# Optimization experiments

Hardware: AMD Instinct MI355X
Metric: run time of the kernel (lower is better)

## Reference

```python
import jax, jax.numpy as jnp
import numpy as np

H = 16  # n_heads
EPS = 1e-12  # F.normalize eps


def _l2norm(x):
    n = jnp.sqrt(jnp.sum(x * x, axis=-1, keepdims=True))
    return x / jnp.maximum(n, EPS)


def setup_inputs() -> dict:
    key = jax.random.key(0)
    ks = jax.random.split(key, 10)
    bs, S, dim = 2, 2048, 2048
    dh = dim // H
    x = jax.random.normal(ks[0], (bs, S, dim), dtype=jnp.float32)
    mask = jnp.ones((bs, S, S), dtype=jnp.int32)  # mask==0 would be masked out
    s = 0.02
    Wq = jax.random.normal(ks[1], (dim, dim), jnp.float32) * s
    bq = jax.random.normal(ks[2], (dim,), jnp.float32) * s
    Wk = jax.random.normal(ks[3], (dim, dim), jnp.float32) * s
    bk = jax.random.normal(ks[4], (dim,), jnp.float32) * s
    Wv = jax.random.normal(ks[5], (dim, dim), jnp.float32) * s
    bv = jax.random.normal(ks[6], (dim,), jnp.float32) * s
    Wo = jax.random.normal(ks[7], (dim, dim), jnp.float32) * s
    bo = jax.random.normal(ks[8], (dim,), jnp.float32) * s
    attention_scale = jnp.asarray(1.0 / np.sqrt(dh), dtype=jnp.float32)
    return {"x": x, "mask": mask, "Wq": Wq, "bq": bq, "Wk": Wk, "bk": bk,
            "Wv": Wv, "bv": bv, "Wo": Wo, "bo": bo,
            "attention_scale": attention_scale}


def reference(x, mask, Wq, bq, Wk, bk, Wv, bv, Wo, bo, attention_scale):
    bs, S, dim = x.shape
    dh = dim // H

    def split_heads(t):  # [bs,S,dim] -> [bs,H,S,dh]
        return t.reshape(bs, S, H, dh).transpose(0, 2, 1, 3)

    q = split_heads(x @ Wq.T + bq)
    k = split_heads(x @ Wk.T + bk)
    v = split_heads(x @ Wv.T + bv)

    # normalized attention: L2-normalize q,k then learned scale on q
    q = _l2norm(q) * attention_scale
    k = _l2norm(k)

    scores = jnp.einsum('bhqd,bhkd->bhqk', q, k)
    masked = mask[:, None, :, :] == 0  # broadcast over heads
    scores = jnp.where(masked, -jnp.inf, scores)
    weights = jax.nn.softmax(scores.astype(jnp.float32), axis=-1).astype(scores.dtype)
    # dropout p=0.0 -> identity
    ctx = jnp.einsum('bhqk,bhkd->bhqd', weights, v)
    ctx = ctx.transpose(0, 2, 1, 3).reshape(bs, S, dim)
    return ctx @ Wo.T + bo
```

## Files before the change

### kernel.cpp

```cpp
#include <hip/hip_runtime.h>
#include <hip/hip_bf16.h>
#include <stdint.h>

typedef __attribute__((ext_vector_type(8))) short short8;
typedef __attribute__((ext_vector_type(4))) float f32x4;
typedef __attribute__((ext_vector_type(4))) unsigned short ushort4v;
typedef __attribute__((ext_vector_type(4))) float float4v;
typedef __attribute__((ext_vector_type(4))) int int4v;

#define GLL16(gp, lp)                                                        \
  __builtin_amdgcn_global_load_lds(                                          \
      (const __attribute__((address_space(1))) void*)(gp),                   \
      (__attribute__((address_space(3))) void*)(lp), 16, 0, 0)

__device__ __forceinline__ unsigned short f2bf(float f) {
  union { float f; unsigned u; } v; v.f = f;
  unsigned r = v.u + 0x7FFFu + ((v.u >> 16) & 1u);
  return (unsigned short)(r >> 16);
}
__device__ __forceinline__ float bf2f(unsigned short h) {
  union { unsigned u; float f; } v; v.u = ((unsigned)h) << 16;
  return v.f;
}
__device__ __forceinline__ unsigned pkbf(float a, float b) {
  union { __hip_bfloat162 h; unsigned u; } v;
  v.h = __float22bfloat162_rn(make_float2(a, b));
  return v.u;
}

__global__ __launch_bounds__(256) void cast_kernel(
    const float* __restrict__ x, const float* __restrict__ Wq,
    const float* __restrict__ Wk, const float* __restrict__ Wv,
    const float* __restrict__ Wo, const float* __restrict__ bq,
    const float* __restrict__ bk, const float* __restrict__ bv,
    unsigned short* __restrict__ xb, unsigned short* __restrict__ wqkv,
    unsigned short* __restrict__ wob, float* __restrict__ biasq) {
  const int X4 = 2097152, W4 = 1048576;
  const int total = X4 + 4 * W4 + 1536;
  for (int i = blockIdx.x * 256 + threadIdx.x; i < total; i += gridDim.x * 256) {
    if (i < X4 + 4 * W4) {
      const float* src; unsigned short* dst;
      if (i < X4) { src = x + (size_t)i * 4; dst = xb + (size_t)i * 4; }
      else {
        int j = i - X4;
        if (j < 3 * W4) {
          const float* w = (j < W4) ? Wq : (j < 2 * W4 ? Wk : Wv);
          int j0 = (j < W4) ? j : (j < 2 * W4 ? j - W4 : j - 2 * W4);
          src = w + (size_t)j0 * 4; dst = wqkv + (size_t)j * 4;
        } else {
          int j0 = j - 3 * W4; src = Wo + (size_t)j0 * 4; dst = wob + (size_t)j0 * 4;
        }
      }
      float4v v = *(const float4v*)src;
      ushort4v o; o.x = f2bf(v.x); o.y = f2bf(v.y); o.z = f2bf(v.z); o.w = f2bf(v.w);
      *(ushort4v*)dst = o;
    } else {
      int j = i - (X4 + 4 * W4);
      const float* src = (j < 512) ? bq + j * 4
                        : (j < 1024 ? bk + (j - 512) * 4 : bv + (j - 1024) * 4);
      *(float4v*)(biasq + j * 4) = *(const float4v*)src;
    }
  }
}

__global__ __launch_bounds__(256) void maskflag_kernel(const int* __restrict__ mask,
                                                       int* __restrict__ flags) {
  const int bid = blockIdx.x;
  const int b = bid >> 9, qt = (bid >> 5) & 15, kt = bid & 31;
  const int t = threadIdx.x;
  const int* mb = mask + (size_t)b * 4194304;
  int ok = 1;
#pragma unroll
  for (int j = 0; j < 8; ++j) {
    int flat = t * 32 + j * 4;
    int r = flat >> 6, c = flat & 63;
    int4v v = *(const int4v*)(mb + (size_t)(qt * 128 + r) * 2048 + kt * 64 + c);
    ok &= (v.x != 0) & (v.y != 0) & (v.z != 0) & (v.w != 0);
  }
  int all = __syncthreads_and(ok);
  if (t == 0) flags[bid] = all;
}

template <bool OUT_BF16>
__global__ __launch_bounds__(256) void gemm_bt(
    const unsigned short* __restrict__ A, const unsigned short* __restrict__ B,
    void* __restrict__ C, const float* __restrict__ bias, int N, int K) {
  __shared__ unsigned short As[128 * 64];
  __shared__ unsigned short Bs[128 * 64];
  const int tid = threadIdx.x, lane = tid & 63;
  const int wid = __builtin_amdgcn_readfirstlane(tid >> 6);
  const int wr = wid >> 1, wc = wid & 1;
  const int bm = blockIdx.y, bn = blockIdx.x;
  const int g = lane >> 4, q15 = lane & 15;
  f32x4 acc[4][4];
#pragma unroll
  for (int i = 0; i < 4; ++i)
#pragma unroll
    for (int j = 0; j < 4; ++j) acc[i][j] = f32x4{0.f, 0.f, 0.f, 0.f};
  const size_t ldab = (size_t)K * 2;
  const int nkt = K >> 6;
  for (int kt = 0; kt < nkt; ++kt) {
#pragma unroll
    for (int i = 0; i < 4; ++i) {
      int c = i * 4 + wid;
      int o = c * 1024 + lane * 16;
      int row = o >> 7, colb = o & 127;
      GLL16((const char*)A + (size_t)(bm * 128 + row) * ldab + kt * 128 + colb,
            (char*)As + c * 1024);
      GLL16((const char*)B + (size_t)(bn * 128 + row) * ldab + kt * 128 + colb,
            (char*)Bs + c * 1024);
    }
    __syncthreads();
#pragma unroll
    for (int kk = 0; kk < 2; ++kk) {
      short8 af[4], bfv[4];
#pragma unroll
      for (int mf = 0; mf < 4; ++mf)
        af[mf] = *(const short8*)((const char*)As +
                 (wr * 64 + mf * 16 + q15) * 128 + kk * 64 + g * 16);
#pragma unroll
      for (int nf = 0; nf < 4; ++nf)
        bfv[nf] = *(const short8*)((const char*)Bs +
                  (wc * 64 + nf * 16 + q15) * 128 + kk * 64 + g * 16);
#pragma unroll
      for (int mf = 0; mf < 4; ++mf)
#pragma unroll
        for (int nf = 0; nf < 4; ++nf)
          acc[mf][nf] = __builtin_amdgcn_mfma_f32_16x16x32_bf16(
              af[mf], bfv[nf], acc[mf][nf], 0, 0, 0);
    }
    __syncthreads();
  }
#pragma unroll
  for (int nf = 0; nf < 4; ++nf) {
    int col = bn * 128 + wc * 64 + nf * 16 + q15;
    float bv = bias[col];
#pragma unroll
    for (int mf = 0; mf < 4; ++mf) {
#pragma unroll
      for (int r = 0; r < 4; ++r) {
        int row = bm * 128 + wr * 64 + mf * 16 + g * 4 + r;
        float v = acc[mf][nf][r] + bv;
        if (OUT_BF16)
          ((unsigned short*)C)[(size_t)row * N + col] = f2bf(v);
        else
          ((float*)C)[(size_t)row * N + col] = v;
      }
    }
  }
}

__global__ __launch_bounds__(256) void norm_vt_kernel(
    unsigned short* __restrict__ QKV, unsigned short* __restrict__ VT,
    const float* __restrict__ scale_p) {
  __shared__ unsigned short vt[128 * 72];
  const int bid = blockIdx.x;
  const int b = bid >> 9, h = (bid >> 5) & 15, st = bid & 31;
  const int t = threadIdx.x;
  const int r = t >> 2, qd = t & 3;
  const float scale = scale_p[0] * 1.4426950408889634f;
  unsigned short* rowp = QKV + (size_t)(b * 2048 + st * 64 + r) * 6144;
#pragma unroll
  for (int part = 0; part < 2; ++part) {
    unsigned short* p = rowp + part * 2048 + h * 128 + qd * 32;
    short8 v[4];
    float ss = 0.f;
#pragma unroll
    for (int j = 0; j < 4; ++j) {
      v[j] = *(const short8*)(p + j * 8);
#pragma unroll
      for (int e = 0; e < 8; ++e) {
        float f = bf2f((unsigned short)v[j][e]);
        ss += f * f;
      }
    }
    ss += __shfl_xor(ss, 1, 64);
    ss += __shfl_xor(ss, 2, 64);
    float inv = 1.0f / fmaxf(sqrtf(ss), 1e-12f);
    if (part == 0) inv *= scale;
#pragma unroll
    for (int j = 0; j < 4; ++j) {
      short8 w;
#pragma unroll
      for (int e = 0; e < 8; ++e)
        w[e] = (short)f2bf(bf2f((unsigned short)v[j][e]) * inv);
      *(short8*)(p + j * 8) = w;
    }
  }
  {
    const unsigned short* p = rowp + 4096 + h * 128 + qd * 32;
#pragma unroll
    for (int j = 0; j < 4; ++j) {
      short8 v = *(const short8*)(p + j * 8);
#pragma unroll
      for (int e = 0; e < 8; ++e) {
        int d = qd * 32 + j * 8 + e;
        vt[d * 72 + r] = (unsigned short)v[e];
      }
    }
  }
  __syncthreads();
  {
    const int d = t >> 1, half = t & 1;
    unsigned short* dst = VT + ((size_t)(b * 16 + h) * 128 + d) * 2048 + st * 64 + half * 32;
#pragma unroll
    for (int j = 0; j < 4; ++j)
      *(short8*)(dst + j * 8) = *(const short8*)(&vt[d * 72 + half * 32 + j * 8]);
  }
}

__global__ __launch_bounds__(512, 4) void flash_kernel(
    const unsigned short* __restrict__ QKV, const unsigned short* __restrict__ VT,
    const int* __restrict__ flags, const int* __restrict__ mask,
    unsigned short* __restrict__ ctx) {
  __shared__ char lds[65536];
  const int tid = threadIdx.x, lane = tid & 63;
  const int wid = __builtin_amdgcn_readfirstlane(tid >> 6);
  const int g = lane >> 4, q15 = lane & 15;
  const int bid = blockIdx.x;
  const int b = bid >> 8, h = (bid >> 4) & 15, qt = bid & 15;

  unsigned fb = 0;
#pragma unroll 1
  for (int i = 0; i < 32; ++i)
    fb |= (unsigned)(flags[b * 512 + qt * 32 + i] != 0) << i;

  short8 qf[4];
  {
    const char* qbase = (const char*)QKV +
        (size_t)(b * 2048 + qt * 128 + wid * 16 + q15) * 12288 + h * 256;
#pragma unroll
    for (int kk = 0; kk < 4; ++kk)
      qf[kk] = *(const short8*)(qbase + kk * 64 + g * 16);
  }

  const char* sptr;
  size_t sbase[4]; int ldso[4]; size_t kstep;
  if (wid < 4) {
    sptr = (const char*)QKV; kstep = (size_t)64 * 12288;
#pragma unroll
    for (int i = 0; i < 4; ++i) {
      int c = wid * 4 + i;
      int row = c * 4 + g;
      int scol = ((lane & 15) * 16) ^ ((row & 7) << 4);
      sbase[i] = (size_t)(b * 2048 + row) * 12288 + 4096 + h * 256 + scol;
      ldso[i] = c * 1024;
    }
  } else {
    sptr = (const char*)VT; kstep = 128;
#pragma unroll
    for (int i = 0; i < 4; ++i) {
      int c2 = (wid - 4) * 4 + i;
      int d = c2 * 8 + (lane >> 3);
      int scol = ((lane & 7) * 16) ^ ((d & 7) << 4);
      sbase[i] = ((size_t)((b * 16 + h) * 128 + d)) * 4096 + scol;
      ldso[i] = 16384 + c2 * 1024;
    }
  }

  f32x4 o[8];
#pragma unroll
  for (int i = 0; i < 8; ++i) o[i] = f32x4{0.f, 0.f, 0.f, 0.f};
  float mrun = -1e30f, lrun = 0.f;
  const int l0 = q15 + 16 * ((2 * g) & 3), l1 = l0 + 16;
  const bool hi = ((g >> 1) & 1) != 0;

#pragma unroll
  for (int i = 0; i < 4; ++i) GLL16(sptr + sbase[i], lds + ldso[i]);
  __syncthreads();

  for (int kt = 0; kt < 32; ++kt) {
    const int cur = kt & 1;
    if (kt < 31) {
#pragma unroll
      for (int i = 0; i < 4; ++i)
        GLL16(sptr + sbase[i] + (size_t)(kt + 1) * kstep,
              lds + (cur ^ 1) * 32768 + ldso[i]);
    }
    const char* Ks = lds + cur * 32768;
    const char* Vs = Ks + 16384;

    f32x4 s[4];
#pragma unroll
    for (int nf = 0; nf < 4; ++nf) s[nf] = f32x4{0.f, 0.f, 0.f, 0.f};
#pragma unroll
    for (int nf = 0; nf < 4; ++nf) {
      const char* kb = Ks + (nf * 16 + q15) * 256;
      const int sw = (q15 & 7) << 4;
#pragma unroll
      for (int kk = 0; kk < 4; ++kk) {
        short8 kf = *(const short8*)(kb + ((kk * 64 + g * 16) ^ sw));
        s[nf] = __builtin_amdgcn_mfma_f32_16x16x32_bf16(kf, qf[kk], s[nf], 0, 0, 0);
      }
    }

    if (!((fb >> kt) & 1)) {
#pragma unroll
      for (int nf = 0; nf < 4; ++nf)
#pragma unroll
        for (int r = 0; r < 4; ++r) {
          int key = kt * 64 + nf * 16 + g * 4 + r;
          int q = qt * 128 + wid * 16 + q15;
          if (mask[(size_t)b * 4194304 + (size_t)q * 2048 + key] == 0)
            s[nf][r] = -__builtin_inff();
        }
    }

    float pmax = s[0][0];
#pragma unroll
    for (int nf = 0; nf < 4; ++nf)
#pragma unroll
      for (int r = 0; r < 4; ++r) pmax = fmaxf(pmax, s[nf][r]);
    pmax = fmaxf(pmax, __shfl_xor(pmax, 16, 64));
    pmax = fmaxf(pmax, __shfl_xor(pmax, 32, 64));

    if (__any(pmax - mrun > 8.0f)) {
      float mnew = fmaxf(mrun, pmax);
      float sc = exp2f(mrun - mnew);
      mrun = mnew; lrun *= sc;
#pragma unroll
      for (int d0 = 0; d0 < 8; ++d0)
#pragma unroll
        for (int r = 0; r < 4; ++r) o[d0][r] *= sc;
    }

    float rs = 0.f;
#pragma unroll
    for (int nf = 0; nf < 4; ++nf)
#pragma unroll
      for (int r = 0; r < 4; ++r) {
        float p = exp2f(s[nf][r] - mrun);
        s[nf][r] = p; rs += p;
      }
    rs += __shfl_xor(rs, 16, 64);
    rs += __shfl_xor(rs, 32, 64);
    lrun += rs;

    unsigned pk[4][2];
#pragma unroll
    for (int nf = 0; nf < 4; ++nf) {
      pk[nf][0] = pkbf(s[nf][0], s[nf][1]);
      pk[nf][1] = pkbf(s[nf][2], s[nf][3]);
    }

#pragma unroll
    for (int kk2 = 0; kk2 < 2; ++kk2) {
      unsigned w0a = __shfl(pk[2*kk2][0], l0, 64), w0b = __shfl(pk[2*kk2+1][0], l0, 64);
      unsigned w1a = __shfl(pk[2*kk2][1], l0, 64), w1b = __shfl(pk[2*kk2+1][1], l0, 64);
      unsigned w2a = __shfl(pk[2*kk2][0], l1, 64), w2b = __shfl(pk[2*kk2+1][0], l1, 64);
      unsigned w3a = __shfl(pk[2*kk2][1], l1, 64), w3b = __shfl(pk[2*kk2+1][1], l1, 64);
      union { unsigned u[4]; short8 s8; } pu;
      pu.u[0] = hi ? w0b : w0a;
      pu.u[1] = hi ? w1b : w1a;
      pu.u[2] = hi ? w2b : w2a;
      pu.u[3] = hi ? w3b : w3a;
#pragma unroll
      for (int d0 = 0; d0 < 8; ++d0) {
        int d = d0 * 16 + q15;
        short8 vf = *(const short8*)(Vs + d * 128 +
                     ((kk2 * 64 + g * 16) ^ ((d & 7) << 4)));
        o[d0] = __builtin_amdgcn_mfma_f32_16x16x32_bf16(vf, pu.s8, o[d0], 0, 0, 0);
      }
    }
    __syncthreads();
  }

  float invl = 1.0f / lrun;
  {
    char* ost = lds;
    int rb = (wid * 16 + q15) * 256;
    int sw = (q15 & 7) << 4;
#pragma unroll
    for (int d0 = 0; d0 < 8; ++d0)
#pragma unroll
      for (int j = 0; j < 2; ++j) {
        unsigned w = pkbf(o[d0][2 * j] * invl, o[d0][2 * j + 1] * invl);
        *(unsigned*)(ost + rb + ((d0 * 32 + g * 8 + j * 4) ^ sw)) = w;
      }
  }
  __syncthreads();
#pragma unroll
  for (int p = 0; p < 4; ++p) {
    int flat = p * 512 + tid;
    int row = flat >> 4, c16 = flat & 15;
    short8 v = *(const short8*)(lds + row * 256 + ((c16 * 16) ^ ((row & 7) << 4)));
    *(short8*)((char*)ctx + (size_t)(b * 2048 + qt * 128 + row) * 4096 +
               h * 256 + c16 * 16) = v;
  }
}

extern "C" void kernel_launch(void* const* d_in, const int* in_sizes, int n_in,
                              void* d_out, int out_size, void* d_ws, size_t ws_size,
                              hipStream_t stream) {
  const float* x  = (const float*)d_in[0];
  const int* mask = (const int*)d_in[1];
  const float* Wq = (const float*)d_in[2];
  const float* bq = (const float*)d_in[3];
  const float* Wk = (const float*)d_in[4];
  const float* bk = (const float*)d_in[5];
  const float* Wv = (const float*)d_in[6];
  const float* bv = (const float*)d_in[7];
  const float* Wo = (const float*)d_in[8];
  const float* bo = (const float*)d_in[9];
  const float* asc = (const float*)d_in[10];

  char* ws = (char*)d_ws;
  unsigned short* xb   = (unsigned short*)(ws);
  unsigned short* wqkv = (unsigned short*)(ws + ((size_t)16 << 20));
  unsigned short* wob  = (unsigned short*)(ws + ((size_t)40 << 20));
  float* biasq         = (float*)(ws + ((size_t)48 << 20));
  int* flags           = (int*)(ws + ((size_t)48 << 20) + (64 << 10));
  unsigned short* qkv  = (unsigned short*)(ws + ((size_t)49 << 20));
  unsigned short* VT   = wqkv;
  unsigned short* ctx  = xb;
  float* out = (float*)d_out;

  hipLaunchKernelGGL(cast_kernel, dim3(2048), dim3(256), 0, stream,
                     x, Wq, Wk, Wv, Wo, bq, bk, bv, xb, wqkv, wob, biasq);
  hipLaunchKernelGGL(maskflag_kernel, dim3(1024), dim3(256), 0, stream, mask, flags);
  hipLaunchKernelGGL((gemm_bt<true>), dim3(48, 32), dim3(256), 0, stream,
                     xb, wqkv, (void*)qkv, biasq, 6144, 2048);
  hipLaunchKernelGGL(norm_vt_kernel, dim3(1024), dim3(256), 0, stream, qkv, VT, asc);
  hipLaunchKernelGGL(flash_kernel, dim3(512), dim3(512), 0, stream,
                     qkv, VT, flags, mask, ctx);
  hipLaunchKernelGGL((gemm_bt<false>), dim3(16, 32), dim3(256), 0, stream,
                     ctx, wob, (void*)out, bo, 2048, 2048);
}
```

Baseline: 490.5 us.

## Replace GEMM with 4-stage pipelined, swizzled 128x256-tile kernel

Replaces the simple single-buffered 128x128 GEMM with a 512-thread kernel using 128x256 tiles and a 4-deep LDS ring of global_load_lds prefetches. Waits are controlled with explicit vmcnt and barriers, and it adds an XOR swizzle on LDS layout to avoid bank conflicts plus setprio around the MFMA bursts. The goal is to hide global memory latency and raise MFMA utilization for the QKV and output projections. In exchange K is hardcoded to 2048 and the kernel uses 96KB of LDS, which limits occupancy.

After: 476.0 us. 1.03x faster.

```diff
diff --git a/kernel.cpp b/kernel.cpp
--- a/kernel.cpp
+++ b/kernel.cpp
@@ -82,58 +82,90 @@
 }
 
 template <bool OUT_BF16>
-__global__ __launch_bounds__(256) void gemm_bt(
+__global__ __launch_bounds__(512, 2) void gemm_p4(
     const unsigned short* __restrict__ A, const unsigned short* __restrict__ B,
-    void* __restrict__ C, const float* __restrict__ bias, int N, int K) {
-  __shared__ unsigned short As[128 * 64];
-  __shared__ unsigned short Bs[128 * 64];
+    void* __restrict__ C, const float* __restrict__ bias, int N) {
+  __shared__ __attribute__((aligned(16))) char lds[98304];
   const int tid = threadIdx.x, lane = tid & 63;
   const int wid = __builtin_amdgcn_readfirstlane(tid >> 6);
-  const int wr = wid >> 1, wc = wid & 1;
+  const int wr = wid >> 2, wc = wid & 3;
+  const int g = lane >> 4, q15 = lane & 15;
   const int bm = blockIdx.y, bn = blockIdx.x;
-  const int g = lane >> 4, q15 = lane & 15;
+  const size_t ldb = 4096;
+
+  const int Rt = tid >> 3;
+  const int wp = ((tid & 7) * 16) ^ ((Rt & 7) << 4);
+  const int sr = Rt * 2 + (wp >> 6), scb = wp & 63;
+  const char* srcA  = (const char*)A + (size_t)(bm * 128 + sr) * ldb + scb;
+  const char* srcB0 = (const char*)B + (size_t)(bn * 256 + sr) * ldb + scb;
+  const char* srcB1 = (const char*)B + (size_t)(bn * 256 + 128 + sr) * ldb + scb;
+  const int dA = tid * 16;
+
+  int aoff[4], boff[4];
+#pragma unroll
+  for (int m = 0; m < 4; ++m) {
+    int r = wr * 64 + m * 16 + q15;
+    aoff[m] = (r >> 1) * 128 + ((((r & 1) << 6) | (g << 4)) ^ (((r >> 1) & 7) << 4));
+    int r2 = wc * 64 + m * 16 + q15;
+    boff[m] = (r2 >> 1) * 128 + ((((r2 & 1) << 6) | (g << 4)) ^ (((r2 >> 1) & 7) << 4));
+  }
+
   f32x4 acc[4][4];
 #pragma unroll
   for (int i = 0; i < 4; ++i)
 #pragma unroll
     for (int j = 0; j < 4; ++j) acc[i][j] = f32x4{0.f, 0.f, 0.f, 0.f};
-  const size_t ldab = (size_t)K * 2;
-  const int nkt = K >> 6;
-  for (int kt = 0; kt < nkt; ++kt) {
-#pragma unroll
-    for (int i = 0; i < 4; ++i) {
-      int c = i * 4 + wid;
-      int o = c * 1024 + lane * 16;
-      int row = o >> 7, colb = o & 127;
-      GLL16((const char*)A + (size_t)(bm * 128 + row) * ldab + kt * 128 + colb,
-            (char*)As + c * 1024);
-      GLL16((const char*)B + (size_t)(bn * 128 + row) * ldab + kt * 128 + colb,
-            (char*)Bs + c * 1024);
-    }
-    __syncthreads();
-#pragma unroll
-    for (int kk = 0; kk < 2; ++kk) {
-      short8 af[4], bfv[4];
-#pragma unroll
-      for (int mf = 0; mf < 4; ++mf)
-        af[mf] = *(const short8*)((const char*)As +
-                 (wr * 64 + mf * 16 + q15) * 128 + kk * 64 + g * 16);
-#pragma unroll
-      for (int nf = 0; nf < 4; ++nf)
-        bfv[nf] = *(const short8*)((const char*)Bs +
-                  (wc * 64 + nf * 16 + q15) * 128 + kk * 64 + g * 16);
-#pragma unroll
-      for (int mf = 0; mf < 4; ++mf)
-#pragma unroll
-        for (int nf = 0; nf < 4; ++nf)
-          acc[mf][nf] = __builtin_amdgcn_mfma_f32_16x16x32_bf16(
-              af[mf], bfv[nf], acc[mf][nf], 0, 0, 0);
-    }
-    __syncthreads();
-  }
+
+#define STAGE(t) do { int d_ = (t) & 3; size_t ko_ = (size_t)(t) * 64;        \
+    GLL16(srcA + ko_, lds + d_ * 8192 + dA);                                  \
+    GLL16(srcB0 + ko_, lds + 32768 + d_ * 16384 + dA);                        \
+    GLL16(srcB1 + ko_, lds + 32768 + d_ * 16384 + 8192 + dA); } while (0)
+
+#define DSR(dst, off) asm volatile("ds_read_b128 %0, %1" : "=v"(dst)          \
+    : "v"((__attribute__((address_space(3))) char*)(lds + (off))))
+
+#define BARX do { __builtin_amdgcn_sched_barrier(0);                          \
+    __builtin_amdgcn_s_barrier(); __builtin_amdgcn_sched_barrier(0); } while (0)
+
+  auto compute = [&](int t) {
+    const int ab = (t & 3) * 8192, bb = 32768 + (t & 3) * 16384;
+    int4v a0, a1, a2, a3, b0, b1, b2, b3;
+    DSR(a0, ab + aoff[0]); DSR(a1, ab + aoff[1]);
+    DSR(a2, ab + aoff[2]); DSR(a3, ab + aoff[3]);
+    DSR(b0, bb + boff[0]); DSR(b1, bb + boff[1]);
+    DSR(b2, bb + boff[2]); DSR(b3, bb + boff[3]);
+    asm volatile("s_waitcnt lgkmcnt(0)" ::: "memory");
+    __builtin_amdgcn_sched_barrier(0);
+    short8 af[4] = {__builtin_bit_cast(short8, a0), __builtin_bit_cast(short8, a1),
+                    __builtin_bit_cast(short8, a2), __builtin_bit_cast(short8, a3)};
+    short8 bf[4] = {__builtin_bit_cast(short8, b0), __builtin_bit_cast(short8, b1),
+                    __builtin_bit_cast(short8, b2), __builtin_bit_cast(short8, b3)};
+    __builtin_amdgcn_s_setprio(1);
+#pragma unroll
+    for (int m = 0; m < 4; ++m)
+#pragma unroll
+      for (int n = 0; n < 4; ++n)
+        acc[m][n] = __builtin_amdgcn_mfma_f32_16x16x32_bf16(af[m], bf[n], acc[m][n], 0, 0, 0);
+    __builtin_amdgcn_s_setprio(0);
+  };
+
+  STAGE(0); STAGE(1); STAGE(2);
+  for (int t = 0; t < 61; ++t) {
+    STAGE(t + 3);
+    asm volatile("s_waitcnt vmcnt(6)" ::: "memory");
+    BARX;
+    compute(t);
+    BARX;
+  }
+  asm volatile("s_waitcnt vmcnt(3)" ::: "memory");
+  BARX; compute(61); BARX;
+  asm volatile("s_waitcnt vmcnt(0)" ::: "memory");
+  BARX; compute(62); BARX;
+  compute(63);
+
 #pragma unroll
   for (int nf = 0; nf < 4; ++nf) {
-    int col = bn * 128 + wc * 64 + nf * 16 + q15;
+    int col = bn * 256 + wc * 64 + nf * 16 + q15;
     float bv = bias[col];
 #pragma unroll
     for (int mf = 0; mf < 4; ++mf) {
@@ -148,6 +180,9 @@
       }
     }
   }
+#undef STAGE
+#undef DSR
+#undef BARX
 }
 
 __global__ __launch_bounds__(256) void norm_vt_kernel(
@@ -418,11 +453,11 @@
   hipLaunchKernelGGL(cast_kernel, dim3(2048), dim3(256), 0, stream,
                      x, Wq, Wk, Wv, Wo, bq, bk, bv, xb, wqkv, wob, biasq);
   hipLaunchKernelGGL(maskflag_kernel, dim3(1024), dim3(256), 0, stream, mask, flags);
-  hipLaunchKernelGGL((gemm_bt<true>), dim3(48, 32), dim3(256), 0, stream,
-                     xb, wqkv, (void*)qkv, biasq, 6144, 2048);
+  hipLaunchKernelGGL((gemm_p4<true>), dim3(24, 32), dim3(512), 0, stream,
+                     xb, wqkv, (void*)qkv, biasq, 6144);
   hipLaunchKernelGGL(norm_vt_kernel, dim3(1024), dim3(256), 0, stream, qkv, VT, asc);
   hipLaunchKernelGGL(flash_kernel, dim3(512), dim3(512), 0, stream,
                      qkv, VT, flags, mask, ctx);
-  hipLaunchKernelGGL((gemm_bt<false>), dim3(16, 32), dim3(256), 0, stream,
-                     ctx, wob, (void*)out, bo, 2048, 2048);
-}
+  hipLaunchKernelGGL((gemm_p4<false>), dim3(8, 32), dim3(512), 0, stream,
+                     ctx, wob, (void*)out, bo, 2048);
+}
```
